# Performance work log

Measured on AMD Instinct MI355X. Metric: run time of the kernel, lower is better.

## Reference

```python
import jax, jax.numpy as jnp
import numpy as np

EMBED = 1024

def setup_inputs() -> dict:
    key = jax.random.key(0)
    ks = jax.random.split(key, 7)
    s = 1.0 / np.sqrt(EMBED)
    x = jax.random.normal(ks[0], (8, 2048, EMBED), dtype=jnp.float32)
    Wk = jax.random.uniform(ks[1], (EMBED, EMBED), jnp.float32, -s, s)
    bk = jax.random.uniform(ks[2], (EMBED,), jnp.float32, -s, s)
    Wq = jax.random.uniform(ks[3], (EMBED, EMBED), jnp.float32, -s, s)
    bq = jax.random.uniform(ks[4], (EMBED,), jnp.float32, -s, s)
    Wv = jax.random.uniform(ks[5], (EMBED, EMBED), jnp.float32, -s, s)
    bv = jax.random.uniform(ks[6], (EMBED,), jnp.float32, -s, s)
    return {"x": x, "Wq": Wq, "bq": bq, "Wk": Wk, "bk": bk, "Wv": Wv, "bv": bv}

def reference(x, Wq, bq, Wk, bk, Wv, bv):
    # Linear projections (PyTorch Linear: y = x @ W^T + b; W here stored as [in, out] = W^T)
    Q = x @ Wq + bq          # [b, s, d]
    K = x @ Wk + bk
    V = x @ Wv + bv
    scale = 1.0 / jnp.sqrt(jnp.asarray(x.shape[-1], x.dtype))
    scores = jnp.einsum('bqd,bkd->bqk', Q, K) * scale  # [b, s, s]
    attn = jax.nn.softmax(scores, axis=-1)
    return jnp.einsum('bqk,bkd->bqd', attn, V)
```

## Files before the change

kernel.cpp:

```cpp
#include <hip/hip_runtime.h>

typedef __attribute__((ext_vector_type(4))) float f32x4;
typedef __attribute__((ext_vector_type(8))) short bf16x8;
typedef __attribute__((ext_vector_type(4))) unsigned short u16x4;

static __device__ __forceinline__ unsigned short f2bf(float f) {
    union { float f; unsigned int u; } a; a.f = f;
    unsigned int u = a.u;
    unsigned int r = (u + 0x7FFFu + ((u >> 16) & 1u)) >> 16;
    return (unsigned short)r;
}
static __device__ __forceinline__ float bf2f(unsigned short h) {
    union { unsigned int u; float f; } a; a.u = ((unsigned int)h) << 16;
    return a.f;
}
static __device__ __forceinline__ unsigned lds_off(const void* p) {
    return (unsigned)(unsigned long long)(const __attribute__((address_space(3))) void*)p;
}

__global__ __launch_bounds__(256) void cvt_f32_bf16(const float* __restrict__ in,
                                                    unsigned short* __restrict__ out) {
    long long i = ((long long)blockIdx.x * 256 + threadIdx.x) * 4;
    float4 f = *(const float4*)(in + i);
    u16x4 u;
    u[0] = f2bf(f.x); u[1] = f2bf(f.y); u[2] = f2bf(f.z); u[3] = f2bf(f.w);
    *(u16x4*)(out + i) = u;
}

__global__ __launch_bounds__(256) void transpose_w(const float* __restrict__ W0,
                                                   const float* __restrict__ W1,
                                                   const float* __restrict__ W2,
                                                   unsigned short* __restrict__ Wt) {
    __shared__ float t[32][33];
    int mat = blockIdx.z;
    const float* W = (mat == 0) ? W0 : (mat == 1) ? W1 : W2;
    unsigned short* out = Wt + (long long)mat * 1024 * 1024;
    int n0 = blockIdx.x * 32, k0 = blockIdx.y * 32;
    int tx = threadIdx.x, ty = threadIdx.y;
#pragma unroll
    for (int q = 0; q < 4; ++q)
        t[ty + 8 * q][tx] = W[(long long)(k0 + ty + 8 * q) * 1024 + n0 + tx];
    __syncthreads();
#pragma unroll
    for (int q = 0; q < 4; ++q)
        out[(long long)(n0 + ty + 8 * q) * 1024 + k0 + tx] = f2bf(t[tx][ty + 8 * q]);
}

#define GBM 256
#define GBN 256

template<int OUT_MODE, int BIAS_MODE>
__global__ __launch_bounds__(512, 2) void gemmpp(
    const unsigned short* __restrict__ A, int lda, long long strideA,
    const unsigned short* __restrict__ B, int ldb, long long strideB,
    void* __restrict__ Cv, int ldc, long long strideC,
    const float* __restrict__ bias, int K, float scale)
{
    __shared__ __align__(16) char lds[131072];

    const int gx = gridDim.x, gy = gridDim.y;
    int lin = blockIdx.x + gx * (blockIdx.y + gy * blockIdx.z);
    const int nwg = gx * gy * gridDim.z;
    const int qch = nwg >> 3;
    int swz = (lin & 7) * qch + (lin >> 3);
    const int bx = swz % gx; int t2 = swz / gx;
    const int by = t2 % gy;  const int bz = t2 / gy;

    const unsigned short* Ag = A + (long long)bz * strideA;
    const unsigned short* Bg = B + (long long)bz * strideB;
    const int m0 = by * GBM, n0 = bx * GBN;

    const int tid  = threadIdx.x;
    const int lane = tid & 63, w = tid >> 6;
    const int wm = w >> 2, wn = w & 3;
    const int l15 = lane & 15, l4 = lane >> 4;

    const int sr = lane >> 3;
    const int ss = (lane & 7) ^ sr;
    const unsigned short* Asrc = Ag + (long long)(m0 + w * 8 + sr) * lda + ss * 8;
    const unsigned short* Bsrc = Bg + (long long)(n0 + w * 8 + sr) * ldb + ss * 8;

    f32x4 acc[8][4] = {};

    auto stageA = [&](int p, int kt, int h) {
#pragma unroll
        for (int i = 0; i < 2; ++i)
            __builtin_amdgcn_global_load_lds(
                (const __attribute__((address_space(1))) void*)(Asrc + (long long)(h * 128 + i * 64) * lda + kt),
                (__attribute__((address_space(3))) void*)(lds + p * 32768 + (h * 128 + i * 64 + w * 8) * 128), 16, 0, 0);
    };
    auto stageB = [&](int p, int kt, int h) {
#pragma unroll
        for (int i = 0; i < 2; ++i)
            __builtin_amdgcn_global_load_lds(
                (const __attribute__((address_space(1))) void*)(Bsrc + (long long)(h * 128 + i * 64) * ldb + kt),
                (__attribute__((address_space(3))) void*)(lds + 65536 + p * 32768 + (h * 128 + i * 64 + w * 8) * 128), 16, 0, 0);
    };

    const unsigned ldsb = lds_off(lds);
    const unsigned as0  = (unsigned)(((l4    ) ^ (l15 & 7)) * 16);
    const unsigned as1  = (unsigned)(((l4 + 4) ^ (l15 & 7)) * 16);
    const unsigned aRow = (unsigned)((wm * 128 + l15) * 128);
    const unsigned bRow = (unsigned)((wn * 64 + l15) * 128);

    bf16x8 aA[4], aB[4], aC[4], aD[4], bA[4], bB[4];
    auto readA = [&](bf16x8 (&af)[4], int p, int mh, int ks) {
        unsigned base = ldsb + (unsigned)(p * 32768) + aRow + (unsigned)(mh * 8192) + (ks ? as1 : as0);
#pragma unroll
        for (int fi = 0; fi < 4; ++fi) {
            unsigned off = base + (unsigned)(fi * 2048);
            asm volatile("ds_read_b128 %0, %1" : "=v"(af[fi]) : "v"(off));
        }
    };
    auto readB = [&](bf16x8 (&bf)[4], int p, int ks) {
        unsigned base = ldsb + 65536u + (unsigned)(p * 32768) + bRow + (ks ? as1 : as0);
#pragma unroll
        for (int nj = 0; nj < 4; ++nj) {
            unsigned off = base + (unsigned)(nj * 2048);
            asm volatile("ds_read_b128 %0, %1" : "=v"(bf[nj]) : "v"(off));
        }
    };
    auto mfma16 = [&](int mh, bf16x8 (&af)[4], bf16x8 (&bf)[4]) {
#pragma unroll
        for (int fi = 0; fi < 4; ++fi)
#pragma unroll
            for (int nj = 0; nj < 4; ++nj)
                acc[mh * 4 + fi][nj] = __builtin_amdgcn_mfma_f32_16x16x32_bf16(
                    af[fi], bf[nj], acc[mh * 4 + fi][nj], 0, 0, 0);
    };

#define VMCNT0 asm volatile("s_waitcnt vmcnt(0)" ::: "memory")
#define LGKM8  asm volatile("s_waitcnt lgkmcnt(8)" ::: "memory")
#define LGKM4  asm volatile("s_waitcnt lgkmcnt(4)" ::: "memory")
#define LGKM0  asm volatile("s_waitcnt lgkmcnt(0)" ::: "memory")
#define SCHED0 __builtin_amdgcn_sched_barrier(0)
#define BARR   __builtin_amdgcn_s_barrier()
#define PRIO1  __builtin_amdgcn_s_setprio(1)
#define PRIO0  __builtin_amdgcn_s_setprio(0)

    const int NT = K >> 6;
    stageA(0, 0, 0); stageA(0, 0, 1); stageB(0, 0, 0); stageB(0, 0, 1);

    for (int t = 0; t < NT; ++t) {
        const int p = t & 1, q = p ^ 1;
        VMCNT0; BARR; SCHED0;
        if (t + 1 < NT) {
            const int kt1 = (t + 1) << 6;
            stageA(q, kt1, 0); stageA(q, kt1, 1);
            stageB(q, kt1, 0); stageB(q, kt1, 1);
        }
        SCHED0;
        readA(aA, p, 0, 0); readB(bA, p, 0);
        readA(aB, p, 1, 0);
        LGKM4; SCHED0; PRIO1; mfma16(0, aA, bA); PRIO0;
        readA(aC, p, 0, 1); readB(bB, p, 1);
        LGKM8; SCHED0; PRIO1; mfma16(1, aB, bA); PRIO0;
        readA(aD, p, 1, 1);
        LGKM4; SCHED0; PRIO1; mfma16(0, aC, bB); PRIO0;
        LGKM0; SCHED0; PRIO1; mfma16(1, aD, bB); PRIO0;
    }

    const float* bias_v = bias;
    asm volatile("" : "+s"(bias_v));
    unsigned short* Cb = (unsigned short*)Cv;
    float* Cf = (float*)Cv;
    long long cbase = (long long)bz * strideC;
#pragma unroll
    for (int mh = 0; mh < 2; ++mh)
#pragma unroll
    for (int fi = 0; fi < 4; ++fi) {
#pragma unroll
        for (int nj = 0; nj < 4; ++nj) {
            int n = n0 + wn * 64 + nj * 16 + l15;
            float bn = (BIAS_MODE == 1) ? bias_v[n] : 0.0f;
#pragma unroll
            for (int r = 0; r < 4; ++r) {
                int m = m0 + wm * 128 + mh * 64 + fi * 16 + l4 * 4 + r;
                float v = acc[mh * 4 + fi][nj][r] * scale + bn;
                if (BIAS_MODE == 2) v += bias_v[m];
                long long idx = cbase + (long long)m * ldc + n;
                if (OUT_MODE == 0) Cb[idx] = f2bf(v);
                else               Cf[idx] = v;
            }
        }
    }
}

__global__ __launch_bounds__(256) void softmax_rows_bf16(unsigned short* __restrict__ S) {
    int row  = blockIdx.x * 4 + (threadIdx.x >> 6);
    int lane = threadIdx.x & 63;
    unsigned short* Srow = S + (long long)row * 2048;
    float v[32];
    float mx = -1e30f;
#pragma unroll
    for (int j = 0; j < 4; ++j) {
        bf16x8 h = *(const bf16x8*)(Srow + j * 512 + lane * 8);
#pragma unroll
        for (int e = 0; e < 8; ++e) {
            float f = bf2f((unsigned short)h[e]);
            v[j * 8 + e] = f;
            mx = fmaxf(mx, f);
        }
    }
#pragma unroll
    for (int o = 32; o; o >>= 1) mx = fmaxf(mx, __shfl_xor(mx, o));
    float sum = 0.0f;
#pragma unroll
    for (int e = 0; e < 32; ++e) {
        v[e] = __expf(v[e] - mx);
        sum += v[e];
    }
#pragma unroll
    for (int o = 32; o; o >>= 1) sum += __shfl_xor(sum, o);
    float inv = 1.0f / sum;
#pragma unroll
    for (int j = 0; j < 4; ++j) {
        bf16x8 h;
#pragma unroll
        for (int e = 0; e < 8; ++e) h[e] = (short)f2bf(v[j * 8 + e] * inv);
        *(bf16x8*)(Srow + j * 512 + lane * 8) = h;
    }
}

extern "C" void kernel_launch(void* const* d_in, const int* in_sizes, int n_in,
                              void* d_out, int out_size, void* d_ws, size_t ws_size,
                              hipStream_t stream) {
    (void)in_sizes; (void)n_in; (void)out_size; (void)ws_size;
    const float* x  = (const float*)d_in[0];
    const float* Wq = (const float*)d_in[1];
    const float* bq = (const float*)d_in[2];
    const float* Wk = (const float*)d_in[3];
    const float* bk = (const float*)d_in[4];
    const float* Wv = (const float*)d_in[5];
    const float* bv = (const float*)d_in[6];

    char* ws = (char*)d_ws;
    unsigned short* Wt  = (unsigned short*)ws;
    unsigned short* Qb  = (unsigned short*)(ws + 6291456);
    unsigned short* Kb  = (unsigned short*)(ws + 39845888);
    unsigned short* Vt  = (unsigned short*)(ws + 73400320);
    unsigned short* xb  = (unsigned short*)(ws + 106954752);
    unsigned short* Sb  = (unsigned short*)(ws + 106954752);

    cvt_f32_bf16<<<dim3(16384), dim3(256), 0, stream>>>(x, xb);
    transpose_w<<<dim3(32, 32, 3), dim3(32, 8), 0, stream>>>(Wq, Wk, Wv, Wt);

    gemmpp<0, 1><<<dim3(4, 64, 1), dim3(512), 0, stream>>>(
        xb, 1024, 0, Wt, 1024, 0, Qb, 1024, 0, bq, 1024, 1.0f);
    gemmpp<0, 1><<<dim3(4, 64, 1), dim3(512), 0, stream>>>(
        xb, 1024, 0, Wt + 1048576, 1024, 0, Kb, 1024, 0, bk, 1024, 1.0f);
    gemmpp<0, 2><<<dim3(64, 4, 1), dim3(512), 0, stream>>>(
        Wt + 2097152, 1024, 0, xb, 1024, 0, Vt, 16384, 0, bv, 1024, 1.0f);

    gemmpp<0, 0><<<dim3(8, 8, 8), dim3(512), 0, stream>>>(
        Qb, 1024, 2097152LL, Kb, 1024, 2097152LL,
        Sb, 2048, 4194304LL, nullptr, 1024, 0.03125f);

    softmax_rows_bf16<<<dim3(4096), dim3(256), 0, stream>>>(Sb);

    gemmpp<1, 0><<<dim3(4, 8, 8), dim3(512), 0, stream>>>(
        Sb, 2048, 4194304LL,
        Vt, 16384, 2048LL,
        d_out, 1024, 2097152LL, nullptr, 2048, 1.0f);
}
```

Baseline: 275.3 us.

## Split global-to-LDS staging into two phases with partial vmcnt waits

Restructures the GEMM main loop so the next tile's B half is staged right after the first barrier and the A half after a second mid-iteration barrier. It waits on vmcnt(2)/vmcnt(4) instead of draining all loads, and reorders the LDS reads and MFMA groups around the split. The aim is to overlap global loads with compute and avoid a full vmcnt(0) stall each iteration, at the cost of an extra barrier per iteration and careful counter reasoning. The kernel is also renamed.

```diff
diff --git a/kernel.cpp b/kernel.cpp
--- a/kernel.cpp
+++ b/kernel.cpp
@@ -50,7 +50,7 @@
 #define GBN 256
 
 template<int OUT_MODE, int BIAS_MODE>
-__global__ __launch_bounds__(512, 2) void gemmpp(
+__global__ __launch_bounds__(512, 2) void gemmcv(
     const unsigned short* __restrict__ A, int lda, long long strideA,
     const unsigned short* __restrict__ B, int ldb, long long strideB,
     void* __restrict__ Cv, int ldc, long long strideC,
@@ -129,6 +129,8 @@
                     af[fi], bf[nj], acc[mh * 4 + fi][nj], 0, 0, 0);
     };
 
+#define VMCNT4 asm volatile("s_waitcnt vmcnt(4)" ::: "memory")
+#define VMCNT2 asm volatile("s_waitcnt vmcnt(2)" ::: "memory")
 #define VMCNT0 asm volatile("s_waitcnt vmcnt(0)" ::: "memory")
 #define LGKM8  asm volatile("s_waitcnt lgkmcnt(8)" ::: "memory")
 #define LGKM4  asm volatile("s_waitcnt lgkmcnt(4)" ::: "memory")
@@ -139,24 +141,23 @@
 #define PRIO0  __builtin_amdgcn_s_setprio(0)
 
     const int NT = K >> 6;
-    stageA(0, 0, 0); stageA(0, 0, 1); stageB(0, 0, 0); stageB(0, 0, 1);
+    stageB(0, 0, 0); stageB(0, 0, 1); stageA(0, 0, 0); stageA(0, 0, 1);
 
     for (int t = 0; t < NT; ++t) {
         const int p = t & 1, q = p ^ 1;
-        VMCNT0; BARR; SCHED0;
-        if (t + 1 < NT) {
-            const int kt1 = (t + 1) << 6;
-            stageA(q, kt1, 0); stageA(q, kt1, 1);
-            stageB(q, kt1, 0); stageB(q, kt1, 1);
-        }
-        SCHED0;
+        const int kt1 = (t + 1) << 6;
+        const bool s1 = (t + 1) < NT;
+        VMCNT2; BARR; SCHED0;
+        if (s1) { stageB(q, kt1, 0); stageB(q, kt1, 1); }
         readA(aA, p, 0, 0); readB(bA, p, 0);
-        readA(aB, p, 1, 0);
-        LGKM4; SCHED0; PRIO1; mfma16(0, aA, bA); PRIO0;
         readA(aC, p, 0, 1); readB(bB, p, 1);
-        LGKM8; SCHED0; PRIO1; mfma16(1, aB, bA); PRIO0;
-        readA(aD, p, 1, 1);
-        LGKM4; SCHED0; PRIO1; mfma16(0, aC, bB); PRIO0;
+        LGKM8; SCHED0; PRIO1; mfma16(0, aA, bA); PRIO0;
+        if (s1) { VMCNT4; } else { VMCNT0; }
+        BARR; SCHED0;
+        if (s1) { stageA(q, kt1, 0); stageA(q, kt1, 1); }
+        readA(aB, p, 1, 0); readA(aD, p, 1, 1);
+        LGKM8; SCHED0; PRIO1; mfma16(0, aC, bB); PRIO0;
+        LGKM4; SCHED0; PRIO1; mfma16(1, aB, bA); PRIO0;
         LGKM0; SCHED0; PRIO1; mfma16(1, aD, bB); PRIO0;
     }
 
@@ -245,20 +246,20 @@
     cvt_f32_bf16<<<dim3(16384), dim3(256), 0, stream>>>(x, xb);
     transpose_w<<<dim3(32, 32, 3), dim3(32, 8), 0, stream>>>(Wq, Wk, Wv, Wt);
 
-    gemmpp<0, 1><<<dim3(4, 64, 1), dim3(512), 0, stream>>>(
+    gemmcv<0, 1><<<dim3(4, 64, 1), dim3(512), 0, stream>>>(
         xb, 1024, 0, Wt, 1024, 0, Qb, 1024, 0, bq, 1024, 1.0f);
-    gemmpp<0, 1><<<dim3(4, 64, 1), dim3(512), 0, stream>>>(
+    gemmcv<0, 1><<<dim3(4, 64, 1), dim3(512), 0, stream>>>(
         xb, 1024, 0, Wt + 1048576, 1024, 0, Kb, 1024, 0, bk, 1024, 1.0f);
-    gemmpp<0, 2><<<dim3(64, 4, 1), dim3(512), 0, stream>>>(
+    gemmcv<0, 2><<<dim3(64, 4, 1), dim3(512), 0, stream>>>(
         Wt + 2097152, 1024, 0, xb, 1024, 0, Vt, 16384, 0, bv, 1024, 1.0f);
 
-    gemmpp<0, 0><<<dim3(8, 8, 8), dim3(512), 0, stream>>>(
+    gemmcv<0, 0><<<dim3(8, 8, 8), dim3(512), 0, stream>>>(
         Qb, 1024, 2097152LL, Kb, 1024, 2097152LL,
         Sb, 2048, 4194304LL, nullptr, 1024, 0.03125f);
 
     softmax_rows_bf16<<<dim3(4096), dim3(256), 0, stream>>>(Sb);
 
-    gemmpp<1, 0><<<dim3(4, 8, 8), dim3(512), 0, stream>>>(
+    gemmcv<1, 0><<<dim3(4, 8, 8), dim3(512), 0, stream>>>(
         Sb, 2048, 4194304LL,
         Vt, 16384, 2048LL,
         d_out, 1024, 2097152LL, nullptr, 2048, 1.0f);
```

After: 278.0 us. No clear change (+1.0%).
